# Optimization experiments

Hardware: AMD Instinct MI355X
Metric: run time of the kernel (lower is better)

Reference implementation:

```python
import jax, jax.numpy as jnp
import numpy as np

N_EMBD = 768
N_HEAD = 12
HEAD_SIZE = N_EMBD // N_HEAD  # 64
WINDOW = 64  # sliding_window_size
EPS = 1e-6


def _rmsnorm(x, g):
    xf = x.astype(jnp.float32)
    n = xf * jax.lax.rsqrt(jnp.mean(xf * xf, axis=-1, keepdims=True) + EPS)
    return n.astype(x.dtype) * g


def _gelu_tanh(x):
    c = jnp.sqrt(jnp.asarray(2.0 / jnp.pi, x.dtype))
    return 0.5 * x * (1.0 + jnp.tanh(c * (x + 0.044715 * x ** 3)))


def setup_inputs() -> dict:
    key = jax.random.key(0)
    ks = jax.random.split(key, 12)
    B, T = 8, 1024
    s = 0.02
    return {
        "x": jax.random.normal(ks[0], (B, T, N_EMBD), jnp.float32),
        "w_q": jax.random.normal(ks[1], (N_EMBD, N_HEAD, HEAD_SIZE), jnp.float32) * s,
        "w_k": jax.random.normal(ks[2], (N_EMBD, N_HEAD, HEAD_SIZE), jnp.float32) * s,
        "w_v": jax.random.normal(ks[3], (N_EMBD, N_HEAD, HEAD_SIZE), jnp.float32) * s,
        "w_proj": jax.random.normal(ks[4], (N_EMBD, N_EMBD), jnp.float32) * s,
        "b_proj": jnp.zeros((N_EMBD,), jnp.float32),
        "w_ff1": jax.random.normal(ks[5], (N_EMBD, 4 * N_EMBD), jnp.float32) * s,
        "b_ff1": jnp.zeros((4 * N_EMBD,), jnp.float32),
        "w_ff2": jax.random.normal(ks[6], (4 * N_EMBD, N_EMBD), jnp.float32) * s,
        "b_ff2": jnp.zeros((N_EMBD,), jnp.float32),
        "g1": jnp.ones((N_EMBD,), jnp.float32),
        "g2": jnp.ones((N_EMBD,), jnp.float32),
    }


def reference(x, w_q, w_k, w_v, w_proj, b_proj, w_ff1, b_ff1, w_ff2, b_ff2, g1, g2):
    B, T, C = x.shape
    # ---- multi-head sliding-window causal attention (eval: dropout = identity) ----
    h = _rmsnorm(x, g1)
    q = jnp.einsum("btc,chd->bhtd", h, w_q)
    k = jnp.einsum("btc,chd->bhtd", h, w_k)
    v = jnp.einsum("btc,chd->bhtd", h, w_v)
    scores = jnp.einsum("bhtd,bhsd->bhts", q, k) / jnp.sqrt(jnp.asarray(HEAD_SIZE, x.dtype))
    pos = jnp.arange(T)
    diff = pos[:, None] - pos[None, :]  # q_pos - k_pos
    mask = (diff < 0) | (diff >= WINDOW)  # causal + sliding window of 64
    scores = jnp.where(mask[None, None], jnp.asarray(-jnp.inf, scores.dtype), scores)
    attn = jax.nn.softmax(scores, axis=-1)
    out = jnp.einsum("bhts,bhsd->bhtd", attn, v)
    out = out.transpose(0, 2, 1, 3).reshape(B, T, C)  # concat heads
    x = x + out @ w_proj + b_proj
    # ---- feedforward ----
    h2 = _rmsnorm(x, g2)
    ff = _gelu_tanh(h2 @ w_ff1 + b_ff1) @ w_ff2 + b_ff2
    x = x + ff
    aux = jnp.asarray(0.0, jnp.float32)
    return (x, aux)
```

## Files before the change

### kernel.cpp

```cpp
#include <hip/hip_runtime.h>
#include <cstdint>

#define DEVI __device__ __forceinline__

typedef __bf16 bf16x8 __attribute__((ext_vector_type(8)));
typedef float  f32x4  __attribute__((ext_vector_type(4)));

template<int V> struct IC { static constexpr int v = V; };

DEVI unsigned short f2b(float f){
  unsigned u = __builtin_bit_cast(unsigned, f);
  unsigned r = u + 0x7FFF + ((u >> 16) & 1);
  return (unsigned short)(r >> 16);
}
DEVI float b2f(unsigned short s){
  unsigned u = ((unsigned)s) << 16;
  return __builtin_bit_cast(float, u);
}
DEVI float gelu_f(float x){
  float u = 0.7978845608028654f * (x + 0.044715f * x * x * x);
  float e = __expf(2.0f * u);
  return x * (1.0f - 1.0f / (e + 1.0f));
}
DEVI void gl_lds16(const unsigned short* g, unsigned short* l){
  __builtin_amdgcn_global_load_lds(
      (const __attribute__((address_space(1))) unsigned int*)g,
      (__attribute__((address_space(3))) unsigned int*)l, 16, 0, 0);
}

__global__ __launch_bounds__(256)
void transpose_f2b(const float* __restrict__ in, unsigned short* __restrict__ out,
                   int R, int C)
{
  __shared__ float tile[32][33];
  int nbx = C >> 5;
  int bx = blockIdx.x % nbx, by = blockIdx.x / nbx;
  int c0 = bx << 5, r0 = by << 5;
  int tx = threadIdx.x & 31, ty = threadIdx.x >> 5;
  #pragma unroll
  for (int j = 0; j < 32; j += 8)
    tile[ty + j][tx] = in[(size_t)(r0 + ty + j) * C + c0 + tx];
  __syncthreads();
  #pragma unroll
  for (int j = 0; j < 32; j += 8)
    out[(size_t)(c0 + ty + j) * R + r0 + tx] = f2b(tile[tx][ty + j]);
}

__global__ __launch_bounds__(256)
void rmsnorm_k(const float* __restrict__ x, const float* __restrict__ g,
               unsigned short* __restrict__ out)
{
  int wid = threadIdx.x >> 6, lane = threadIdx.x & 63;
  size_t row = (size_t)blockIdx.x * 4 + wid;
  const float* xr = x + row * 768;
  float4 v[3];
  float ss = 0.0f;
  #pragma unroll
  for (int c = 0; c < 3; c++){
    v[c] = *(const float4*)&xr[lane * 4 + c * 256];
    ss += v[c].x * v[c].x + v[c].y * v[c].y + v[c].z * v[c].z + v[c].w * v[c].w;
  }
  #pragma unroll
  for (int o = 32; o >= 1; o >>= 1) ss += __shfl_xor(ss, o);
  float rs = rsqrtf(ss * (1.0f / 768.0f) + 1e-6f);
  #pragma unroll
  for (int c = 0; c < 3; c++){
    const float4 gv = *(const float4*)&g[lane * 4 + c * 256];
    ushort4 o4;
    o4.x = f2b(v[c].x * rs * gv.x);
    o4.y = f2b(v[c].y * rs * gv.y);
    o4.z = f2b(v[c].z * rs * gv.z);
    o4.w = f2b(v[c].w * rs * gv.w);
    *(ushort4*)&out[row * 768 + lane * 4 + c * 256] = o4;
  }
}

template<int BM, bool BIAS, bool GELU_, bool RES, bool OUTF32>
__global__ __launch_bounds__(256, BM == 64 ? 3 : 2)
void gemm_db(const unsigned short* __restrict__ A, const unsigned short* __restrict__ Bt,
             const float* __restrict__ bias, const float* __restrict__ res,
             void* __restrict__ outp, int M, int N, int K)
{
  constexpr int MI = BM / 32;
  constexpr int AL = (BM * 8) / 256;
  constexpr int BUFSZ = (BM + 128) * 64;
  __shared__ unsigned short sm[2][BUFSZ];

  int tid = threadIdx.x, wid = tid >> 6, lane = tid & 63;
  int la = lane & 15, hi = lane >> 4;
  int wm = wid >> 1, wn = wid & 1;
  int tiles_n = N >> 7;
  int bid = blockIdx.x;
  bid = (bid & 7) * (gridDim.x >> 3) + (bid >> 3);
  int m0 = (bid / tiles_n) * BM, n0 = (bid % tiles_n) << 7;
  int NT = K >> 6;

  f32x4 acc[MI][4] = {};

  const unsigned short* aSrc[AL];
  const unsigned short* bSrc[4];
  unsigned short* aDst[2][AL];
  unsigned short* bDst[2][4];
  #pragma unroll
  for (int l = 0; l < AL; l++){
    int cb = wid * (BM * 2) + l * 64;
    int idx = cb + lane;
    int row = idx >> 3, sl2 = (idx & 7) ^ (row & 7);
    aSrc[l] = A + (size_t)(m0 + row) * K + sl2 * 8;
    aDst[0][l] = &sm[0][cb * 8];
    aDst[1][l] = &sm[1][cb * 8];
  }
  #pragma unroll
  for (int l = 0; l < 4; l++){
    int cb = wid * 256 + l * 64;
    int idx = cb + lane;
    int row = idx >> 3, sl2 = (idx & 7) ^ (row & 7);
    bSrc[l] = Bt + (size_t)(n0 + row) * K + sl2 * 8;
    bDst[0][l] = &sm[0][BM * 64 + cb * 8];
    bDst[1][l] = &sm[1][BM * 64 + cb * 8];
  }

  const unsigned short* fa[2][2];
  const unsigned short* fb[2][2];
  #pragma unroll
  for (int bf = 0; bf < 2; bf++)
    #pragma unroll
    for (int kk = 0; kk < 2; kk++){
      int sw = (((kk * 4 + hi) ^ (la & 7))) * 8;
      fa[bf][kk] = &sm[bf][(wm * (BM / 2) + la) * 64 + sw];
      fb[bf][kk] = &sm[bf][BM * 64 + (wn * 64 + la) * 64 + sw];
    }

  auto stageTo = [&](auto BF){
    constexpr int bf = decltype(BF)::v;
    #pragma unroll
    for (int l = 0; l < AL; l++){ gl_lds16(aSrc[l], aDst[bf][l]); aSrc[l] += 64; }
    #pragma unroll
    for (int l = 0; l < 4; l++){ gl_lds16(bSrc[l], bDst[bf][l]); bSrc[l] += 64; }
  };

  stageTo(IC<0>{});

  auto tile_step = [&](auto BUF, int t){
    constexpr int CB = decltype(BUF)::v;
    if (t + 1 < NT){
      stageTo(IC<CB ^ 1>{});
      if constexpr (BM == 128) asm volatile("s_waitcnt vmcnt(8)" ::: "memory");
      else                     asm volatile("s_waitcnt vmcnt(6)" ::: "memory");
    } else {
      asm volatile("s_waitcnt vmcnt(0)" ::: "memory");
    }
    __builtin_amdgcn_s_barrier();

    bf16x8 afr[MI][2], bfr[4][2];
    #pragma unroll
    for (int mm = 0; mm < MI; mm++){
      afr[mm][0] = *(const bf16x8*)(fa[CB][0] + mm * 1024);
      afr[mm][1] = *(const bf16x8*)(fa[CB][1] + mm * 1024);
    }
    #pragma unroll
    for (int nn = 0; nn < 4; nn++){
      bfr[nn][0] = *(const bf16x8*)(fb[CB][0] + nn * 1024);
      bfr[nn][1] = *(const bf16x8*)(fb[CB][1] + nn * 1024);
    }
    __builtin_amdgcn_s_setprio(1);
    #pragma unroll
    for (int mm = 0; mm < MI; mm++)
      #pragma unroll
      for (int nn = 0; nn < 4; nn++)
        #pragma unroll
        for (int kk = 0; kk < 2; kk++)
          acc[mm][nn] = __builtin_amdgcn_mfma_f32_16x16x32_bf16(
              afr[mm][kk], bfr[nn][kk], acc[mm][nn], 0, 0, 0);
    __builtin_amdgcn_s_setprio(0);

    __builtin_amdgcn_s_barrier();
  };

  for (int t = 0; t < NT; t += 2){
    tile_step(IC<0>{}, t);
    tile_step(IC<1>{}, t + 1);
  }

  float* outF = (float*)outp;
  unsigned short* outB = (unsigned short*)outp;
  #pragma unroll
  for (int mm = 0; mm < MI; mm++){
    int rowb = m0 + wm * (BM / 2) + mm * 16 + hi * 4;
    #pragma unroll
    for (int nn = 0; nn < 4; nn++){
      int col = n0 + wn * 64 + nn * 16 + la;
      float bv = BIAS ? bias[col] : 0.0f;
      #pragma unroll
      for (int r = 0; r < 4; r++){
        float val = acc[mm][nn][r] + bv;
        if (GELU_) val = gelu_f(val);
        if (RES)   val += res[(size_t)(rowb + r) * N + col];
        size_t o = (size_t)(rowb + r) * N + col;
        if (OUTF32) outF[o] = val;
        else        outB[o] = f2b(val);
      }
    }
  }
}

__global__ __launch_bounds__(256)
void attn_k(const unsigned short* __restrict__ qkv, unsigned short* __restrict__ attn)
{
  __shared__ unsigned short Qs[64 * 72];
  __shared__ unsigned short Ks[128 * 72];
  __shared__ unsigned short Vt[64 * 136];
  __shared__ unsigned short Ps[4][16 * 136];

  int tid = threadIdx.x, wid = tid >> 6, lane = tid & 63;
  int la = lane & 15, hi = lane >> 4;
  int blk = blockIdx.x;
  blk = (blk & 7) * (gridDim.x >> 3) + (blk >> 3);
  int tile = blk & 15, hb = blk >> 4;
  int h = hb % 12, b = hb / 12;
  int t0 = tile << 6;

  const unsigned short* qbase = qkv + (size_t)(b * 1024) * 2304 + h * 64;

  #pragma unroll
  for (int r = 0; r < 2; r++){
    int idx = tid + r * 256;
    int row = idx >> 3, ch = idx & 7;
    uint4 v = *(const uint4*)(qbase + (size_t)(t0 + row) * 2304 + ch * 8);
    *(uint4*)&Qs[row * 72 + ch * 8] = v;
  }
  #pragma unroll
  for (int r = 0; r < 4; r++){
    int idx = tid + r * 256;
    int row = idx >> 3, ch = idx & 7;
    int sg = t0 - 64 + row; sg = sg < 0 ? 0 : sg;
    uint4 v = *(const uint4*)(qbase + 768 + (size_t)sg * 2304 + ch * 8);
    *(uint4*)&Ks[row * 72 + ch * 8] = v;
  }
  #pragma unroll
  for (int r = 0; r < 4; r++){
    int idx = tid + r * 256;
    int s = idx & 127, ch = idx >> 7;
    int sg = t0 - 64 + s; sg = sg < 0 ? 0 : sg;
    uint4 v = *(const uint4*)(qbase + 1536 + (size_t)sg * 2304 + ch * 8);
    unsigned short tmp[8];
    *(uint4*)tmp = v;
    #pragma unroll
    for (int j = 0; j < 8; j++)
      Vt[(ch * 8 + j) * 136 + s] = tmp[j];
  }
  __syncthreads();

  f32x4 sc[8];
  #pragma unroll
  for (int sj = 0; sj < 8; sj++) sc[sj] = (f32x4){0.f, 0.f, 0.f, 0.f};
  #pragma unroll
  for (int kk = 0; kk < 2; kk++){
    bf16x8 aq = *(const bf16x8*)&Qs[(wid * 16 + la) * 72 + kk * 32 + hi * 8];
    #pragma unroll
    for (int sj = 0; sj < 8; sj++){
      bf16x8 bk = *(const bf16x8*)&Ks[(sj * 16 + la) * 72 + kk * 32 + hi * 8];
      sc[sj] = __builtin_amdgcn_mfma_f32_16x16x32_bf16(aq, bk, sc[sj], 0, 0, 0);
    }
  }

  float inv[4];
  #pragma unroll
  for (int r2 = 0; r2 < 4; r2++){
    int row = wid * 16 + hi * 4 + r2;
    float mx = -1e30f;
    #pragma unroll
    for (int sj = 0; sj < 8; sj++){
      int sl = sj * 16 + la;
      bool valid = (sl >= row + 1) && (sl <= row + 64) && (t0 - 64 + sl >= 0);
      float sv = valid ? sc[sj][r2] * 0.125f : -1e30f;
      sc[sj][r2] = sv;
      mx = fmaxf(mx, sv);
    }
    #pragma unroll
    for (int o = 8; o >= 1; o >>= 1) mx = fmaxf(mx, __shfl_xor(mx, o));
    float sum = 0.0f;
    #pragma unroll
    for (int sj = 0; sj < 8; sj++){
      float p = __expf(sc[sj][r2] - mx);
      sc[sj][r2] = p;
      sum += p;
    }
    #pragma unroll
    for (int o = 8; o >= 1; o >>= 1) sum += __shfl_xor(sum, o);
    inv[r2] = 1.0f / sum;
  }

  unsigned short* myP = Ps[wid];
  #pragma unroll
  for (int sj = 0; sj < 8; sj++)
    #pragma unroll
    for (int r2 = 0; r2 < 4; r2++)
      myP[(hi * 4 + r2) * 136 + sj * 16 + la] = f2b(sc[sj][r2]);

  __syncthreads();

  f32x4 oacc[4];
  #pragma unroll
  for (int nj = 0; nj < 4; nj++) oacc[nj] = (f32x4){0.f, 0.f, 0.f, 0.f};
  #pragma unroll
  for (int ks = 0; ks < 4; ks++){
    bf16x8 ap = *(const bf16x8*)&myP[la * 136 + ks * 32 + hi * 8];
    #pragma unroll
    for (int nj = 0; nj < 4; nj++){
      bf16x8 bv = *(const bf16x8*)&Vt[(nj * 16 + la) * 136 + ks * 32 + hi * 8];
      oacc[nj] = __builtin_amdgcn_mfma_f32_16x16x32_bf16(ap, bv, oacc[nj], 0, 0, 0);
    }
  }

  unsigned short* obase = attn + (size_t)(b * 1024 + t0) * 768 + h * 64;
  #pragma unroll
  for (int nj = 0; nj < 4; nj++)
    #pragma unroll
    for (int r2 = 0; r2 < 4; r2++){
      int row = wid * 16 + hi * 4 + r2;
      obase[(size_t)row * 768 + nj * 16 + la] = f2b(oacc[nj][r2] * inv[r2]);
    }
}

__global__ void aux_k(float* p){ if (threadIdx.x == 0) p[0] = 0.0f; }

extern "C" void kernel_launch(void* const* d_in, const int* in_sizes, int n_in,
                              void* d_out, int out_size, void* d_ws, size_t ws_size,
                              hipStream_t stream)
{
  const float* x      = (const float*)d_in[0];
  const float* w_q    = (const float*)d_in[1];
  const float* w_k    = (const float*)d_in[2];
  const float* w_v    = (const float*)d_in[3];
  const float* w_proj = (const float*)d_in[4];
  const float* b_proj = (const float*)d_in[5];
  const float* w_ff1  = (const float*)d_in[6];
  const float* b_ff1  = (const float*)d_in[7];
  const float* w_ff2  = (const float*)d_in[8];
  const float* b_ff2  = (const float*)d_in[9];
  const float* g1     = (const float*)d_in[10];
  const float* g2     = (const float*)d_in[11];
  float* out = (float*)d_out;

  char* ws = (char*)d_ws;
  size_t off = 0;
  auto alloc = [&](size_t bytes){ size_t r = off; off += (bytes + 255) & ~(size_t)255; return r; };
  const size_t BT = 8 * 1024;

  unsigned short* h     = (unsigned short*)(ws + alloc(BT * 768 * 2));
  unsigned short* qkv   = (unsigned short*)(ws + alloc(BT * 3072 * 2));
  float*          x2    = (float*)         (ws + alloc(BT * 768 * 4));
  unsigned short* h2    = (unsigned short*)(ws + alloc(BT * 768 * 2));
  unsigned short* WqkvT = (unsigned short*)(ws + alloc(2304 * 768 * 2));
  unsigned short* WprojT= (unsigned short*)(ws + alloc(768 * 768 * 2));
  unsigned short* Wff1T = (unsigned short*)(ws + alloc(3072 * 768 * 2));
  unsigned short* Wff2T = (unsigned short*)(ws + alloc(768 * 3072 * 2));
  unsigned short* attn  = h;
  unsigned short* ffa   = qkv;

  transpose_f2b<<<576, 256, 0, stream>>>(w_q,    WqkvT,             768, 768);
  transpose_f2b<<<576, 256, 0, stream>>>(w_k,    WqkvT + 768 * 768, 768, 768);
  transpose_f2b<<<576, 256, 0, stream>>>(w_v,    WqkvT + 1536 * 768,768, 768);
  transpose_f2b<<<576, 256, 0, stream>>>(w_proj, WprojT,            768, 768);
  transpose_f2b<<<24 * 96, 256, 0, stream>>>(w_ff1, Wff1T, 768, 3072);
  transpose_f2b<<<96 * 24, 256, 0, stream>>>(w_ff2, Wff2T, 3072, 768);

  rmsnorm_k<<<2048, 256, 0, stream>>>(x, g1, h);

  gemm_db<128,false,false,false,false><<<64 * 18, 256, 0, stream>>>(h, WqkvT, nullptr, nullptr, qkv, 8192, 2304, 768);

  attn_k<<<8 * 12 * 16, 256, 0, stream>>>(qkv, attn);

  gemm_db<64,true,false,true,true><<<128 * 6, 256, 0, stream>>>(attn, WprojT, b_proj, x, x2, 8192, 768, 768);

  rmsnorm_k<<<2048, 256, 0, stream>>>(x2, g2, h2);

  gemm_db<128,true,true,false,false><<<64 * 24, 256, 0, stream>>>(h2, Wff1T, b_ff1, nullptr, ffa, 8192, 3072, 768);

  gemm_db<64,true,false,true,true><<<128 * 6, 256, 0, stream>>>(ffa, Wff2T, b_ff2, x2, out, 8192, 768, 3072);

  aux_k<<<1, 64, 0, stream>>>(out + 6291456);
}
```

Before: 220.7 us.

## Add 256x256-tile 8-wave GEMM kernel for QKV and FF1 projections

Introduces a new GEMM kernel with 256x256 output tiles, 512 threads (8 waves each owning 128x64), double-buffered swizzled LDS staging, and set-priority around the MFMA clusters. It replaces the 128-row gemm_db for the QKV and FF1 projections. The larger tiles are meant to raise arithmetic intensity and cut global/LDS traffic per FLOP. The cost is 128KB of LDS per block and large accumulator register pressure, plus fewer blocks (288 and 384) relative to the CU count, which can leave some CUs underused.

```diff
diff --git a/kernel.cpp b/kernel.cpp
--- a/kernel.cpp
+++ b/kernel.cpp
@@ -72,6 +72,129 @@
     o4.z = f2b(v[c].z * rs * gv.z);
     o4.w = f2b(v[c].w * rs * gv.w);
     *(ushort4*)&out[row * 768 + lane * 4 + c * 256] = o4;
+  }
+}
+
+template<bool BIAS, bool GELU_, bool OUTF32>
+__global__ __launch_bounds__(512, 2)
+void gemm256(const unsigned short* __restrict__ A, const unsigned short* __restrict__ Bt,
+             const float* __restrict__ bias, void* __restrict__ outp,
+             int M, int N, int K)
+{
+  __shared__ unsigned short sm[2][32768];
+  int tid = threadIdx.x, wid = tid >> 6, lane = tid & 63;
+  int la = lane & 15, hi = lane >> 4;
+  int wm = wid >> 2, wn = wid & 3;
+  int tiles_n = N >> 8;
+  int bid = blockIdx.x;
+  bid = (bid & 7) * (gridDim.x >> 3) + (bid >> 3);
+  int m0 = (bid / tiles_n) << 8, n0 = (bid % tiles_n) << 8;
+  int NT = K >> 6;
+
+  f32x4 acc[8][4] = {};
+
+  const unsigned short* aSrc[4];
+  const unsigned short* bSrc[4];
+  unsigned short* aDst[2][4];
+  unsigned short* bDst[2][4];
+  #pragma unroll
+  for (int l = 0; l < 4; l++){
+    int cb = l * 512 + wid * 64;
+    int idx = cb + lane;
+    int row = idx >> 3, sl2 = (idx & 7) ^ (row & 7);
+    aSrc[l] = A + (size_t)(m0 + row) * K + sl2 * 8;
+    bSrc[l] = Bt + (size_t)(n0 + row) * K + sl2 * 8;
+    aDst[0][l] = &sm[0][cb * 8];            aDst[1][l] = &sm[1][cb * 8];
+    bDst[0][l] = &sm[0][16384 + cb * 8];    bDst[1][l] = &sm[1][16384 + cb * 8];
+  }
+
+  const unsigned short* fA[2][2];
+  const unsigned short* fB[2][2];
+  #pragma unroll
+  for (int bf = 0; bf < 2; bf++)
+    #pragma unroll
+    for (int kk = 0; kk < 2; kk++){
+      int sw = ((kk * 4 + hi) ^ (la & 7)) * 8;
+      fA[bf][kk] = &sm[bf][(wm * 128 + la) * 64 + sw];
+      fB[bf][kk] = &sm[bf][16384 + (wn * 64 + la) * 64 + sw];
+    }
+
+  auto stageTo = [&](auto BF){
+    constexpr int bf = decltype(BF)::v;
+    #pragma unroll
+    for (int l = 0; l < 4; l++){ gl_lds16(aSrc[l], aDst[bf][l]); aSrc[l] += 64; }
+    #pragma unroll
+    for (int l = 0; l < 4; l++){ gl_lds16(bSrc[l], bDst[bf][l]); bSrc[l] += 64; }
+  };
+
+  stageTo(IC<0>{});
+
+  auto tile_step = [&](auto BUF, int t){
+    constexpr int CB = decltype(BUF)::v;
+    if (t + 1 < NT){
+      stageTo(IC<CB ^ 1>{});
+      asm volatile("s_waitcnt vmcnt(8)" ::: "memory");
+    } else {
+      asm volatile("s_waitcnt vmcnt(0)" ::: "memory");
+    }
+    __builtin_amdgcn_s_barrier();
+
+    bf16x8 bfr[4][2];
+    #pragma unroll
+    for (int p = 0; p < 4; p++){
+      bf16x8 afr[2][2];
+      #pragma unroll
+      for (int mi = 0; mi < 2; mi++){
+        afr[mi][0] = *(const bf16x8*)(fA[CB][0] + (p * 2 + mi) * 1024);
+        afr[mi][1] = *(const bf16x8*)(fA[CB][1] + (p * 2 + mi) * 1024);
+      }
+      if (p == 0){
+        #pragma unroll
+        for (int nn = 0; nn < 4; nn++){
+          bfr[nn][0] = *(const bf16x8*)(fB[CB][0] + nn * 1024);
+          bfr[nn][1] = *(const bf16x8*)(fB[CB][1] + nn * 1024);
+        }
+      }
+      __builtin_amdgcn_s_barrier();
+      asm volatile("s_waitcnt lgkmcnt(0)" ::: "memory");
+      __builtin_amdgcn_sched_barrier(0);
+      __builtin_amdgcn_s_setprio(1);
+      #pragma unroll
+      for (int mi = 0; mi < 2; mi++)
+        #pragma unroll
+        for (int nn = 0; nn < 4; nn++)
+          #pragma unroll
+          for (int kk = 0; kk < 2; kk++)
+            acc[p * 2 + mi][nn] = __builtin_amdgcn_mfma_f32_16x16x32_bf16(
+                afr[mi][kk], bfr[nn][kk], acc[p * 2 + mi][nn], 0, 0, 0);
+      __builtin_amdgcn_s_setprio(0);
+      __builtin_amdgcn_s_barrier();
+    }
+  };
+
+  for (int t = 0; t < NT; t += 2){
+    tile_step(IC<0>{}, t);
+    tile_step(IC<1>{}, t + 1);
+  }
+
+  float* outF = (float*)outp;
+  unsigned short* outB = (unsigned short*)outp;
+  #pragma unroll
+  for (int mm = 0; mm < 8; mm++){
+    int rowb = m0 + wm * 128 + mm * 16 + hi * 4;
+    #pragma unroll
+    for (int nn = 0; nn < 4; nn++){
+      int col = n0 + wn * 64 + nn * 16 + la;
+      float bv = BIAS ? bias[col] : 0.0f;
+      #pragma unroll
+      for (int r = 0; r < 4; r++){
+        float val = acc[mm][nn][r] + bv;
+        if (GELU_) val = gelu_f(val);
+        size_t o = (size_t)(rowb + r) * N + col;
+        if (OUTF32) outF[o] = val;
+        else        outB[o] = f2b(val);
+      }
+    }
   }
 }
 
@@ -368,7 +491,7 @@
 
   rmsnorm_k<<<2048, 256, 0, stream>>>(x, g1, h);
 
-  gemm_db<128,false,false,false,false><<<64 * 18, 256, 0, stream>>>(h, WqkvT, nullptr, nullptr, qkv, 8192, 2304, 768);
+  gemm256<false,false,false><<<32 * 9, 512, 0, stream>>>(h, WqkvT, nullptr, qkv, 8192, 2304, 768);
 
   attn_k<<<8 * 12 * 16, 256, 0, stream>>>(qkv, attn);
 
@@ -376,7 +499,7 @@
 
   rmsnorm_k<<<2048, 256, 0, stream>>>(x2, g2, h2);
 
-  gemm_db<128,true,true,false,false><<<64 * 24, 256, 0, stream>>>(h2, Wff1T, b_ff1, nullptr, ffa, 8192, 3072, 768);
+  gemm256<true,true,false><<<32 * 12, 512, 0, stream>>>(h2, Wff1T, b_ff1, ffa, 8192, 3072, 768);
 
   gemm_db<64,true,false,true,true><<<128 * 6, 256, 0, stream>>>(ffa, Wff2T, b_ff2, x2, out, 8192, 768, 3072);
 
```

New measurement: 246.4 us. 1.12x slower.
